# Performance work log

Measured on AMD Instinct MI355X. Metric: run time of the kernel, lower is better.

Reference implementation:

```python
import jax, jax.numpy as jnp
import numpy as np

RPE_LEN = 14  # rpe_length
HEADS = 10
HDIM = 64
EMBED = 640
DFF = 2560


def layer_norm(x, g, b, eps=1e-5):
    mu = jnp.mean(x, axis=-1, keepdims=True)
    var = jnp.var(x, axis=-1, keepdims=True)
    return (x - mu) * jax.lax.rsqrt(var + eps) * g + b


def rpe_embeddings(table_v, table_h, N):
    """RelativePosition2D.forward(N, N) -> [N, N, head_dim]."""
    L = N - 1
    s = int(L ** 0.5)  # 14 for N=197
    r = jnp.arange(L)
    dist_v = r[None, :] // s - r[:, None] // s
    dist_h = r[None, :] % s - r[:, None] % s
    idx_v = jnp.clip(dist_v, -RPE_LEN, RPE_LEN) + RPE_LEN + 1
    idx_h = jnp.clip(dist_h, -RPE_LEN, RPE_LEN) + RPE_LEN + 1
    # pad one row/col of zeros at the front (class token -> index 0)
    idx_v = jnp.pad(idx_v, ((1, 0), (1, 0)))
    idx_h = jnp.pad(idx_h, ((1, 0), (1, 0)))
    return table_v[idx_v] + table_h[idx_h]


def setup_inputs() -> dict:
    key = jax.random.key(0)
    ks = jax.random.split(key, 20)
    B, N, E, H, D, F = 64, 197, EMBED, HEADS, HDIM, DFF
    T = 2 * RPE_LEN + 2  # 30
    std = 0.02
    return {
        "x": jax.random.normal(ks[0], (B, N, E), jnp.float32),
        "ln1_g": jnp.ones((E,), jnp.float32),
        "ln1_b": jnp.zeros((E,), jnp.float32),
        "Wq": jax.random.normal(ks[1], (H * D, E), jnp.float32) * std,
        "Wk": jax.random.normal(ks[2], (H * D, E), jnp.float32) * std,
        "Wv": jax.random.normal(ks[3], (H * D, E), jnp.float32) * std,
        "Wp": jax.random.normal(ks[4], (E, H * D), jnp.float32) * std,
        "bp": jnp.zeros((E,), jnp.float32),
        "rpk_v": jax.random.normal(ks[5], (T, D), jnp.float32) * std,
        "rpk_h": jax.random.normal(ks[6], (T, D), jnp.float32) * std,
        "rpv_v": jax.random.normal(ks[7], (T, D), jnp.float32) * std,
        "rpv_h": jax.random.normal(ks[8], (T, D), jnp.float32) * std,
        "ln2_g": jnp.ones((E,), jnp.float32),
        "ln2_b": jnp.zeros((E,), jnp.float32),
        "W1": jax.random.normal(ks[9], (F, E), jnp.float32) * std,
        "b1": jnp.zeros((F,), jnp.float32),
        "W2": jax.random.normal(ks[10], (E, F), jnp.float32) * std,
        "b2": jnp.zeros((E,), jnp.float32),
    }


def reference(x, ln1_g, ln1_b, Wq, Wk, Wv, Wp, bp,
              rpk_v, rpk_h, rpv_v, rpv_h,
              ln2_g, ln2_b, W1, b1, W2, b2):
    B, N, E = x.shape
    H, D = HEADS, HDIM
    scale = D ** (-0.5)

    # --- attention block (pre-norm) ---
    residual = x
    h = layer_norm(x, ln1_g, ln1_b)
    q = (h @ Wq.T).reshape(B, N, H, D)
    k = (h @ Wk.T).reshape(B, N, H, D)
    v = (h @ Wv.T).reshape(B, N, H, D)

    attn = jnp.einsum('bnhd,bmhd->bhnm', q, k) * scale
    r_p_k = rpe_embeddings(rpk_v, rpk_h, N)          # [N, N, D]
    attn = attn + jnp.einsum('bnhd,nmd->bhnm', q, r_p_k) * scale
    attn = jax.nn.softmax(attn, axis=-1)

    o = jnp.einsum('bhnm,bmhd->bhnd', attn, v)
    r_p_v = rpe_embeddings(rpv_v, rpv_h, N)          # [N, N, D]
    o = o + jnp.einsum('bhnm,nmd->bhnd', attn, r_p_v)
    o = o.transpose(0, 2, 1, 3).reshape(B, N, H * D)
    x = residual + o @ Wp.T + bp

    # --- FFN block (pre-norm) ---
    residual = x
    h = layer_norm(x, ln2_g, ln2_b)
    h = jax.nn.gelu(h @ W1.T + b1, approximate=False)
    x = residual + h @ W2.T + b2
    return x
```

## Files before the change

kernel.cpp:

```cpp
#include <hip/hip_runtime.h>
#include <hip/hip_bf16.h>
#include <math.h>

#define NN   197
#define EE   640
#define HH   10
#define DD   64
#define FF   2560
#define MTOK (64 * 197)
#define RPE_T 30

typedef __hip_bfloat16 bf16;
typedef __attribute__((ext_vector_type(8))) __bf16 bf16x8;
typedef __attribute__((ext_vector_type(4))) float  floatx4;
typedef __attribute__((ext_vector_type(8))) unsigned short ushort8;

#define MFMA32(a, b, c) __builtin_amdgcn_mfma_f32_16x16x32_bf16(a, b, c, 0, 0, 0)

__device__ __forceinline__ float bfbits2f(unsigned short u) {
    union { unsigned int i; float f; } x; x.i = ((unsigned int)u) << 16; return x.f;
}
__device__ __forceinline__ unsigned short f2bf(float f) {
    bf16 t = __float2bfloat16(f);
    unsigned short u; __builtin_memcpy(&u, &t, 2); return u;
}
__device__ __forceinline__ void gld16(const bf16* g, bf16* l) {
    __builtin_amdgcn_global_load_lds(
        (const __attribute__((address_space(1))) unsigned int*)g,
        (__attribute__((address_space(3))) unsigned int*)l, 16, 0, 0);
}

__global__ void detect_kernel(const unsigned int* __restrict__ g, int* __restrict__ flag) {
    if (threadIdx.x == 0) flag[0] = (g[0] == 0x3F800000u) ? 1 : 0;
}

struct ConvDesc {
    const void* src[18];
    bf16*       dst[18];
    int         end8[18];
};

__global__ __launch_bounds__(256) void conv_fused(
    ConvDesc d, int total8, const int* __restrict__ flag)
{
    int c = blockIdx.x * 256 + threadIdx.x;
    if (c >= total8) return;
    int s = 0, start = 0;
#pragma unroll
    for (int i = 0; i < 17; ++i) {
        if (c >= d.end8[i]) { s = i + 1; start = d.end8[i]; }
    }
    int local = c - start;
    if (flag[0]) {
        const float* sp = (const float*)d.src[s] + (size_t)local * 8;
        bf16 t[8];
#pragma unroll
        for (int j = 0; j < 8; ++j) t[j] = __float2bfloat16(sp[j]);
        *(ushort8*)(d.dst[s] + (size_t)local * 8) = *(const ushort8*)t;
    } else {
        ((ushort8*)d.dst[s])[local] = ((const ushort8*)d.src[s])[local];
    }
}

__global__ __launch_bounds__(256) void rpetrans_kernel(
    const bf16* __restrict__ rvv, const bf16* __restrict__ rvh,
    unsigned short* __restrict__ rvvT, unsigned short* __restrict__ rvhT)
{
    int t = blockIdx.x * 256 + threadIdx.x;
    if (t < 64 * 32) {
        int d = t >> 5, tt = t & 31;
        rvvT[t] = (tt < RPE_T) ? ((const unsigned short*)rvv)[tt * 64 + d] : 0;
        rvhT[t] = (tt < RPE_T) ? ((const unsigned short*)rvh)[tt * 64 + d] : 0;
    }
}

__global__ __launch_bounds__(256) void vtrans_kernel(
    const bf16* __restrict__ qkv, unsigned short* __restrict__ VtG)
{
    int bh = blockIdx.x;
    int b = bh / HH, h = bh % HH;
    unsigned short* dst = VtG + (size_t)bh * (64 * 224);
    for (int t = threadIdx.x; t < 224 * 8; t += 256) {
        int m = t >> 3, d8 = (t & 7) << 3;
        ushort8 val = {0, 0, 0, 0, 0, 0, 0, 0};
        if (m < NN)
            val = *(const ushort8*)(qkv + ((size_t)b * NN + m) * 1920 + 1280 + h * 64 + d8);
#pragma unroll
        for (int j = 0; j < 8; ++j) dst[(d8 + j) * 224 + m] = val[j];
    }
}

__global__ __launch_bounds__(256) void ln_kernel(
    const void* __restrict__ xb, size_t xrow0, int xdyn,
    const int* __restrict__ flag,
    const bf16* __restrict__ g, const bf16* __restrict__ b,
    bf16* __restrict__ out, int nrows)
{
    int row  = blockIdx.x * 4 + (threadIdx.x >> 6);
    if (row >= nrows) return;
    int lane = threadIdx.x & 63;
    const int f32 = xdyn && flag[0];
    const size_t base = (xrow0 + row) * (size_t)EE;
    float vals[10];
    float s = 0.f, ss = 0.f;
#pragma unroll
    for (int j = 0; j < 10; ++j) {
        int e = j * 64 + lane;
        float f = f32 ? ((const float*)xb)[base + e]
                      : (float)((const bf16*)xb)[base + e];
        vals[j] = f; s += f; ss += f * f;
    }
#pragma unroll
    for (int off = 32; off; off >>= 1) {
        s  += __shfl_xor(s, off);
        ss += __shfl_xor(ss, off);
    }
    float mean = s * (1.f / EE);
    float var  = ss * (1.f / EE) - mean * mean;
    float rs   = rsqrtf(var + 1e-5f);
#pragma unroll
    for (int j = 0; j < 10; ++j) {
        int e = j * 64 + lane;
        float hv = (vals[j] - mean) * rs * (float)g[e] + (float)b[e];
        out[(size_t)row * EE + e] = __float2bfloat16(hv);
    }
}

__global__ __launch_bounds__(256) void gemm128(
    const bf16* __restrict__ A, const bf16* __restrict__ B,
    const bf16* __restrict__ bias,
    const void* __restrict__ residb, size_t resid_row0, int resid_dyn,
    void* __restrict__ outb, size_t out_row0, int out_dyn,
    const int* __restrict__ flag,
    int M, int N, int K, int gelu)
{
    __shared__ bf16 At[2][128 * 32];
    __shared__ bf16 Bt[2][128 * 32];

    const int tid  = threadIdx.x;
    const int wave = tid >> 6, lane = tid & 63;
    const int quad = lane >> 4, l16 = lane & 15;
    const int wy = wave >> 1, wx = wave & 1;
    const int n0 = blockIdx.x * 128;
    const int m0 = blockIdx.y * 128;

    const int drow   = wave * 16 + (lane >> 2);
    const int gchunk = ((lane & 3) ^ ((lane >> 3) & 3)) * 8;
    const int ar0 = min(m0 + drow, M - 1);
    const int ar1 = min(m0 + 64 + drow, M - 1);
    const bf16* Ag0 = A + (size_t)ar0 * K + gchunk;
    const bf16* Ag1 = A + (size_t)ar1 * K + gchunk;
    const bf16* Bg0 = B + (size_t)(n0 + drow) * K + gchunk;
    const bf16* Bg1 = B + (size_t)(n0 + 64 + drow) * K + gchunk;
    bf16* At00 = &At[0][wave * 512];
    bf16* At01 = &At[0][2048 + wave * 512];
    bf16* At10 = &At[1][wave * 512];
    bf16* At11 = &At[1][2048 + wave * 512];
    bf16* Bt00 = &Bt[0][wave * 512];
    bf16* Bt01 = &Bt[0][2048 + wave * 512];
    bf16* Bt10 = &Bt[1][wave * 512];
    bf16* Bt11 = &Bt[1][2048 + wave * 512];

    const int swz = (quad ^ ((l16 >> 1) & 3)) * 8;

    floatx4 acc[4][4] = {};

    for (int k0 = 0; k0 < K; k0 += 64) {
        __syncthreads();
        gld16(Ag0 + k0,      At00);
        gld16(Ag1 + k0,      At01);
        gld16(Ag0 + k0 + 32, At10);
        gld16(Ag1 + k0 + 32, At11);
        gld16(Bg0 + k0,      Bt00);
        gld16(Bg1 + k0,      Bt01);
        gld16(Bg0 + k0 + 32, Bt10);
        gld16(Bg1 + k0 + 32, Bt11);
        __syncthreads();

#pragma unroll
        for (int kk = 0; kk < 2; ++kk) {
            bf16x8 af[4], bfr[4];
#pragma unroll
            for (int s = 0; s < 4; ++s)
                af[s] = *(const bf16x8*)(&At[kk][(wy * 64 + s * 16 + l16) * 32 + swz]);
#pragma unroll
            for (int t = 0; t < 4; ++t)
                bfr[t] = *(const bf16x8*)(&Bt[kk][(wx * 64 + t * 16 + l16) * 32 + swz]);
#pragma unroll
            for (int s = 0; s < 4; ++s)
#pragma unroll
                for (int t = 0; t < 4; ++t)
                    acc[s][t] = MFMA32(af[s], bfr[t], acc[s][t]);
        }
    }

    const int fr = resid_dyn && flag[0];
    const int fo = out_dyn && flag[0];
    float bv[4];
#pragma unroll
    for (int t = 0; t < 4; ++t)
        bv[t] = bias ? (float)bias[n0 + wx * 64 + t * 16 + l16] : 0.f;

#pragma unroll
    for (int s = 0; s < 4; ++s) {
#pragma unroll
        for (int i = 0; i < 4; ++i) {
            int m = m0 + wy * 64 + s * 16 + quad * 4 + i;
            if (m < M) {
                size_t rowoff_o = (out_row0 + m) * (size_t)N;
                size_t rowoff_r = (resid_row0 + m) * (size_t)N;
#pragma unroll
                for (int t = 0; t < 4; ++t) {
                    int n = n0 + wx * 64 + t * 16 + l16;
                    float v = acc[s][t][i] + bv[t];
                    if (gelu) v = 0.5f * v * (1.f + erff(v * 0.70710678118f));
                    if (residb)
                        v += fr ? ((const float*)residb)[rowoff_r + n]
                                : (float)((const bf16*)residb)[rowoff_r + n];
                    if (fo) ((float*)outb)[rowoff_o + n] = v;
                    else    ((bf16*)outb)[rowoff_o + n]  = __float2bfloat16(v);
                }
            }
        }
    }
}

__global__ __launch_bounds__(256) void attn_kernel(
    const bf16* __restrict__ qkv,
    const bf16* __restrict__ tkv, const bf16* __restrict__ tkh,
    const unsigned short* __restrict__ rvvT,
    const unsigned short* __restrict__ rvhT,
    const unsigned short* __restrict__ VtG,
    bf16* __restrict__ o)
{
    __shared__ unsigned short Pm[64 * 232];
    __shared__ unsigned short PSv[64 * 40];
    __shared__ unsigned short PSh[64 * 40];
    __shared__ float QTv[64 * 32];
    __shared__ float QTh[64 * 32];

    const int tid  = threadIdx.x;
    const int wave = tid >> 6, lane = tid & 63;
    const int quad = lane >> 4, l16 = lane & 15;
    const int b  = blockIdx.x / HH, h = blockIdx.x % HH;
    const int qt = blockIdx.y;
    const size_t rowbase = (size_t)b * NN;

    for (int t = tid; t < 64 * 40; t += 256) { PSv[t] = 0; PSh[t] = 0; }
    for (int t = tid; t < 64 * 24; t += 256) Pm[(t / 24) * 232 + 208 + (t % 24)] = 0;
    __syncthreads();

    const int rA = qt * 64 + wave * 16 + l16;
    const bf16* qrow = qkv + (rowbase + min(rA, NN - 1)) * 1920 + h * 64;
    bf16x8 qa0 = *(const bf16x8*)(qrow + quad * 8);
    bf16x8 qa1 = *(const bf16x8*)(qrow + 32 + quad * 8);

    {
        floatx4 av[2] = {}, ah[2] = {};
#pragma unroll
        for (int ct = 0; ct < 2; ++ct) {
            int t = min(ct * 16 + l16, RPE_T - 1);
            av[ct] = MFMA32(qa0, *(const bf16x8*)(tkv + t * 64 + quad * 8), av[ct]);
            av[ct] = MFMA32(qa1, *(const bf16x8*)(tkv + t * 64 + 32 + quad * 8), av[ct]);
            ah[ct] = MFMA32(qa0, *(const bf16x8*)(tkh + t * 64 + quad * 8), ah[ct]);
            ah[ct] = MFMA32(qa1, *(const bf16x8*)(tkh + t * 64 + 32 + quad * 8), ah[ct]);
        }
#pragma unroll
        for (int ct = 0; ct < 2; ++ct)
#pragma unroll
            for (int i = 0; i < 4; ++i) {
                int row = wave * 16 + quad * 4 + i;
                QTv[row * 32 + ct * 16 + l16] = av[ct][i];
                QTh[row * 32 + ct * 16 + l16] = ah[ct][i];
            }
    }

    floatx4 sacc[13];
#pragma unroll
    for (int mt = 0; mt < 13; ++mt) {
        const bf16* krow = qkv + (rowbase + min(mt * 16 + l16, NN - 1)) * 1920
                           + 640 + h * 64;
        floatx4 a = {};
        a = MFMA32(qa0, *(const bf16x8*)(krow + quad * 8), a);
        a = MFMA32(qa1, *(const bf16x8*)(krow + 32 + quad * 8), a);
        sacc[mt] = a;
    }

    int nn4[4], jn4[4], in4[4];
#pragma unroll
    for (int i = 0; i < 4; ++i) {
        int n = qt * 64 + wave * 16 + quad * 4 + i;
        nn4[i] = n;
        jn4[i] = (n > 0) ? (n - 1) / 14 : 0;
        in4[i] = (n > 0) ? (n - 1) % 14 : 0;
    }
    float mx4[4] = {-3e38f, -3e38f, -3e38f, -3e38f};
#pragma unroll
    for (int mt = 0; mt < 13; ++mt) {
        int m = mt * 16 + l16;
        int jm = (m > 0) ? (m - 1) / 14 : 0;
        int im = (m > 0) ? (m - 1) % 14 : 0;
        bool mok = (m < NN);
#pragma unroll
        for (int i = 0; i < 4; ++i) {
            int row = wave * 16 + quad * 4 + i;
            int iv = (nn4[i] == 0 || m == 0) ? 0 : (jm - jn4[i] + 15);
            int ih = (nn4[i] == 0 || m == 0) ? 0 : (im - in4[i] + 15);
            float val = mok ? (sacc[mt][i] + QTv[row * 32 + iv] + QTh[row * 32 + ih]) * 0.125f
                            : -3e38f;
            sacc[mt][i] = val;
            mx4[i] = fmaxf(mx4[i], val);
        }
    }
#pragma unroll
    for (int i = 0; i < 4; ++i)
#pragma unroll
        for (int off = 1; off < 16; off <<= 1)
            mx4[i] = fmaxf(mx4[i], __shfl_xor(mx4[i], off));

    float sm4[4] = {0.f, 0.f, 0.f, 0.f};
#pragma unroll
    for (int mt = 0; mt < 13; ++mt) {
#pragma unroll
        for (int i = 0; i < 4; ++i) {
            float p = __expf(sacc[mt][i] - mx4[i]);
            sm4[i] += p;
            Pm[(wave * 16 + quad * 4 + i) * 232 + mt * 16 + l16] = f2bf(p);
        }
    }
#pragma unroll
    for (int i = 0; i < 4; ++i)
#pragma unroll
        for (int off = 1; off < 16; off <<= 1)
            sm4[i] += __shfl_xor(sm4[i], off);

    for (int t = lane; t < 224; t += 64) {
        int rl = t / 14, j = t % 14;
        int row = wave * 16 + rl;
        int n = qt * 64 + row;
        if (n >= 1 && n < NN) {
            float aR = 0.f, aC = 0.f;
#pragma unroll
            for (int u = 0; u < 14; ++u) {
                aR += bfbits2f(Pm[row * 232 + 1 + j * 14 + u]);
                aC += bfbits2f(Pm[row * 232 + 1 + u * 14 + j]);
            }
            int jn2 = (n - 1) / 14, in2 = (n - 1) % 14;
            PSv[row * 40 + (j - jn2 + 15)] = f2bf(aR);
            PSh[row * 40 + (j - in2 + 15)] = f2bf(aC);
        }
    }
    if (lane < 16) {
        int row = wave * 16 + lane;
        int n = qt * 64 + row;
        if (n < NN) {
            float p0 = (n == 0) ? sm4[0] : bfbits2f(Pm[row * 232]);
            PSv[row * 40] = f2bf(p0);
            PSh[row * 40] = f2bf(p0);
        }
    }

    floatx4 oacc[4] = {};
    {
        bf16x8 pav = *(const bf16x8*)(const void*)&PSv[(wave * 16 + l16) * 40 + quad * 8];
        bf16x8 pah = *(const bf16x8*)(const void*)&PSh[(wave * 16 + l16) * 40 + quad * 8];
#pragma unroll
        for (int ct = 0; ct < 4; ++ct) {
            bf16x8 bv  = *(const bf16x8*)(const void*)&rvvT[(ct * 16 + l16) * 32 + quad * 8];
            bf16x8 bh2 = *(const bf16x8*)(const void*)&rvhT[(ct * 16 + l16) * 32 + quad * 8];
            oacc[ct] = MFMA32(pav, bv,  oacc[ct]);
            oacc[ct] = MFMA32(pah, bh2, oacc[ct]);
        }
    }
    const unsigned short* vt = VtG + (size_t)blockIdx.x * (64 * 224);
    for (int k0 = 0; k0 < 224; k0 += 32) {
        bf16x8 pa = *(const bf16x8*)(const void*)&Pm[(wave * 16 + l16) * 232 + k0 + quad * 8];
#pragma unroll
        for (int ct = 0; ct < 4; ++ct) {
            bf16x8 vb = *(const bf16x8*)(const void*)&vt[(ct * 16 + l16) * 224 + k0 + quad * 8];
            oacc[ct] = MFMA32(pa, vb, oacc[ct]);
        }
    }
#pragma unroll
    for (int i = 0; i < 4; ++i) {
        float rinv = 1.f / sm4[i];
        int row = wave * 16 + quad * 4 + i;
        int n = qt * 64 + row;
        if (n < NN) {
#pragma unroll
            for (int ct = 0; ct < 4; ++ct)
                o[(rowbase + n) * 640 + h * 64 + ct * 16 + l16] =
                    __float2bfloat16(oacc[ct][i] * rinv);
        }
    }
}

extern "C" void kernel_launch(void* const* d_in, const int* in_sizes, int n_in,
                              void* d_out, int out_size, void* d_ws, size_t ws_size,
                              hipStream_t stream)
{
    char* ws = (char*)d_ws;
    size_t off = 0;
    auto alloc = [&](size_t bytes) -> void* {
        void* p = ws + off;
        off += (bytes + 255) & ~(size_t)255;
        return p;
    };

    int* flag = (int*)alloc(256);
    bf16* xc   = (bf16*)alloc((size_t)MTOK * EE * 2);
    bf16* Wqc  = (bf16*)alloc((size_t)EE * EE * 2);
    bf16* Wkc  = (bf16*)alloc((size_t)EE * EE * 2);
    bf16* Wvc  = (bf16*)alloc((size_t)EE * EE * 2);
    bf16* Wpc  = (bf16*)alloc((size_t)EE * EE * 2);
    bf16* W1c  = (bf16*)alloc((size_t)FF * EE * 2);
    bf16* W2c  = (bf16*)alloc((size_t)EE * FF * 2);
    bf16* l1g  = (bf16*)alloc(EE * 2);
    bf16* l1b  = (bf16*)alloc(EE * 2);
    bf16* l2g  = (bf16*)alloc(EE * 2);
    bf16* l2b  = (bf16*)alloc(EE * 2);
    bf16* bpc  = (bf16*)alloc(EE * 2);
    bf16* b1c  = (bf16*)alloc(FF * 2);
    bf16* b2c  = (bf16*)alloc(EE * 2);
    bf16* rkv  = (bf16*)alloc(RPE_T * DD * 2);
    bf16* rkh  = (bf16*)alloc(RPE_T * DD * 2);
    bf16* rvv  = (bf16*)alloc(RPE_T * DD * 2);
    bf16* rvh  = (bf16*)alloc(RPE_T * DD * 2);
    unsigned short* rvvT = (unsigned short*)alloc(64 * 32 * 2);
    unsigned short* rvhT = (unsigned short*)alloc(64 * 32 * 2);
    const size_t cvt_end = off;

    int Bc = 0;
    const int cands[6] = {64, 32, 16, 8, 4, 2};
    for (int i = 0; i < 6; ++i) {
        size_t rows = (size_t)NN * cands[i];
        size_t need = cvt_end + rows * 10240 + (size_t)cands[i] * HH * 64 * 224 * 2 + 8192;
        if (need <= ws_size) { Bc = cands[i]; break; }
    }
    if (Bc == 0) return;

    const int nchunks = 64 / Bc;
    const int rows    = NN * Bc;
    bf16* h1   = (bf16*)alloc((size_t)rows * EE * 2);
    bf16* qkvb = (bf16*)alloc((size_t)rows * 1920 * 2);
    bf16* h3   = (bf16*)alloc((size_t)rows * FF * 2);
    unsigned short* VtG = (unsigned short*)alloc((size_t)Bc * HH * 64 * 224 * 2);

    detect_kernel<<<1, 64, 0, stream>>>((const unsigned int*)d_in[1], flag);
    {
        ConvDesc cd;
        const void* srcs[18] = { d_in[0], d_in[3], d_in[4], d_in[5], d_in[6],
                                 d_in[14], d_in[16], d_in[1], d_in[2], d_in[12],
                                 d_in[13], d_in[7], d_in[15], d_in[17], d_in[8],
                                 d_in[9], d_in[10], d_in[11] };
        bf16* dsts[18] = { xc, Wqc, Wkc, Wvc, Wpc, W1c, W2c, l1g, l1b, l2g,
                           l2b, bpc, b1c, b2c, rkv, rkh, rvv, rvh };
        int ns[18] = { MTOK * EE, EE * EE, EE * EE, EE * EE, EE * EE, FF * EE,
                       EE * FF, EE, EE, EE, EE, EE, FF, EE,
                       RPE_T * DD, RPE_T * DD, RPE_T * DD, RPE_T * DD };
        int cum = 0;
        for (int i = 0; i < 18; ++i) {
            cd.src[i] = srcs[i]; cd.dst[i] = dsts[i];
            cum += ns[i] / 8; cd.end8[i] = cum;
        }
        conv_fused<<<(cum + 255) / 256, 256, 0, stream>>>(cd, cum, flag);
    }
    rpetrans_kernel<<<8, 256, 0, stream>>>(rvv, rvh, rvvT, rvhT);

    const int gM128 = (rows + 127) / 128;
    const int gLN   = (rows + 3) / 4;

    for (int c = 0; c < nchunks; ++c) {
        const size_t row0 = (size_t)c * rows;

        ln_kernel<<<gLN, 256, 0, stream>>>(xc, row0, 0, flag, l1g, l1b, h1, rows);

        gemm128<<<dim3(1920 / 128, gM128), 256, 0, stream>>>(
            h1, Wqc, nullptr, nullptr, 0, 0, qkvb, 0, 0, flag, rows, 1920, EE, 0);

        vtrans_kernel<<<Bc * HH, 256, 0, stream>>>(qkvb, VtG);

        attn_kernel<<<dim3(Bc * HH, 4), 256, 0, stream>>>(
            qkvb, rkv, rkh, rvvT, rvhT, VtG, h1);

        gemm128<<<dim3(EE / 128, gM128), 256, 0, stream>>>(
            h1, Wpc, bpc, xc, row0, 0, d_out, row0, 1, flag, rows, EE, EE, 0);
    }

    for (int c = 0; c < nchunks; ++c) {
        const size_t row0 = (size_t)c * rows;

        ln_kernel<<<gLN, 256, 0, stream>>>(d_out, row0, 1, flag, l2g, l2b, h1, rows);

        gemm128<<<dim3(FF / 128, gM128), 256, 0, stream>>>(
            h1, W1c, b1c, nullptr, 0, 0, h3, 0, 0, flag, rows, FF, EE, 1);

        gemm128<<<dim3(EE / 128, gM128), 256, 0, stream>>>(
            h3, W2c, b2c, d_out, row0, 1, d_out, row0, 1, flag, rows, EE, FF, 0);
    }
}
```

Baseline: 503.5 us.

## Compute RPE value sums via MFMA selection matrices, tanh GELU, swap GEMM grid order

Replaces the scalar row/column summation of attention probabilities (used for the relative-position value term) with MFMA products against precomputed 0/1 selection matrices, fused into the P·V loop. Stores the Q·RPE-key tables in bf16 instead of fp32 in shared memory. Swaps the exact erf GELU for a tanh approximation built on exp. Swaps the GEMM grid axes so M tiles vary fastest, changing L2 reuse of weight tiles. The tanh GELU and the bf16 tables add approximation error.

```diff
diff --git a/kernel.cpp b/kernel.cpp
--- a/kernel.cpp
+++ b/kernel.cpp
@@ -29,6 +29,14 @@
         (const __attribute__((address_space(1))) unsigned int*)g,
         (__attribute__((address_space(3))) unsigned int*)l, 16, 0, 0);
 }
+__device__ __forceinline__ float gelu_f(float v) {
+    float y = 0.7978845608f * (v + 0.044715f * v * v * v);
+    float a = fabsf(y);
+    float e = __expf(-2.f * a);
+    float t = (1.f - e) / (1.f + e);
+    t = (y < 0.f) ? -t : t;
+    return 0.5f * v * (1.f + t);
+}
 
 __global__ void detect_kernel(const unsigned int* __restrict__ g, int* __restrict__ flag) {
     if (threadIdx.x == 0) flag[0] = (g[0] == 0x3F800000u) ? 1 : 0;
@@ -71,6 +79,18 @@
         int d = t >> 5, tt = t & 31;
         rvvT[t] = (tt < RPE_T) ? ((const unsigned short*)rvv)[tt * 64 + d] : 0;
         rvhT[t] = (tt < RPE_T) ? ((const unsigned short*)rvh)[tt * 64 + d] : 0;
+    }
+}
+
+__global__ __launch_bounds__(256) void selbuild_kernel(
+    bf16* __restrict__ SelV, bf16* __restrict__ SelH)
+{
+    int t = blockIdx.x * 256 + threadIdx.x;
+    if (t < 16 * 224) {
+        int j = t / 224, m = t % 224;
+        bool valid = (j < 14) && (m >= 1) && (m < 197);
+        SelV[t] = __float2bfloat16((valid && (m - 1) / 14 == j) ? 1.f : 0.f);
+        SelH[t] = __float2bfloat16((valid && (m - 1) % 14 == j) ? 1.f : 0.f);
     }
 }
 
@@ -141,8 +161,8 @@
     const int wave = tid >> 6, lane = tid & 63;
     const int quad = lane >> 4, l16 = lane & 15;
     const int wy = wave >> 1, wx = wave & 1;
-    const int n0 = blockIdx.x * 128;
-    const int m0 = blockIdx.y * 128;
+    const int m0 = blockIdx.x * 128;
+    const int n0 = blockIdx.y * 128;
 
     const int drow   = wave * 16 + (lane >> 2);
     const int gchunk = ((lane & 3) ^ ((lane >> 3) & 3)) * 8;
@@ -213,7 +233,7 @@
                 for (int t = 0; t < 4; ++t) {
                     int n = n0 + wx * 64 + t * 16 + l16;
                     float v = acc[s][t][i] + bv[t];
-                    if (gelu) v = 0.5f * v * (1.f + erff(v * 0.70710678118f));
+                    if (gelu) v = gelu_f(v);
                     if (residb)
                         v += fr ? ((const float*)residb)[rowoff_r + n]
                                 : (float)((const bf16*)residb)[rowoff_r + n];
@@ -231,13 +251,14 @@
     const unsigned short* __restrict__ rvvT,
     const unsigned short* __restrict__ rvhT,
     const unsigned short* __restrict__ VtG,
+    const bf16* __restrict__ SelV, const bf16* __restrict__ SelH,
     bf16* __restrict__ o)
 {
     __shared__ unsigned short Pm[64 * 232];
     __shared__ unsigned short PSv[64 * 40];
     __shared__ unsigned short PSh[64 * 40];
-    __shared__ float QTv[64 * 32];
-    __shared__ float QTh[64 * 32];
+    __shared__ unsigned short QTv[64 * 32];
+    __shared__ unsigned short QTh[64 * 32];
 
     const int tid  = threadIdx.x;
     const int wave = tid >> 6, lane = tid & 63;
@@ -270,8 +291,8 @@
 #pragma unroll
             for (int i = 0; i < 4; ++i) {
                 int row = wave * 16 + quad * 4 + i;
-                QTv[row * 32 + ct * 16 + l16] = av[ct][i];
-                QTh[row * 32 + ct * 16 + l16] = ah[ct][i];
+                QTv[row * 32 + ct * 16 + l16] = f2bf(av[ct][i]);
+                QTh[row * 32 + ct * 16 + l16] = f2bf(ah[ct][i]);
             }
     }
 
@@ -306,7 +327,8 @@
             int row = wave * 16 + quad * 4 + i;
             int iv = (nn4[i] == 0 || m == 0) ? 0 : (jm - jn4[i] + 15);
             int ih = (nn4[i] == 0 || m == 0) ? 0 : (im - in4[i] + 15);
-            float val = mok ? (sacc[mt][i] + QTv[row * 32 + iv] + QTh[row * 32 + ih]) * 0.125f
+            float val = mok ? (sacc[mt][i] + bfbits2f(QTv[row * 32 + iv])
+                               + bfbits2f(QTh[row * 32 + ih])) * 0.125f
                             : -3e38f;
             sacc[mt][i] = val;
             mx4[i] = fmaxf(mx4[i], val);
@@ -334,20 +356,28 @@
         for (int off = 1; off < 16; off <<= 1)
             sm4[i] += __shfl_xor(sm4[i], off);
 
-    for (int t = lane; t < 224; t += 64) {
-        int rl = t / 14, j = t % 14;
-        int row = wave * 16 + rl;
+    floatx4 oacc[4] = {};
+    floatx4 psv = {}, psh = {};
+    const unsigned short* vt = VtG + (size_t)blockIdx.x * (64 * 224);
+    for (int k0 = 0; k0 < 224; k0 += 32) {
+        bf16x8 pa = *(const bf16x8*)(const void*)&Pm[(wave * 16 + l16) * 232 + k0 + quad * 8];
+#pragma unroll
+        for (int ct = 0; ct < 4; ++ct) {
+            bf16x8 vb = *(const bf16x8*)(const void*)&vt[(ct * 16 + l16) * 224 + k0 + quad * 8];
+            oacc[ct] = MFMA32(pa, vb, oacc[ct]);
+        }
+        psv = MFMA32(pa, *(const bf16x8*)(SelV + l16 * 224 + k0 + quad * 8), psv);
+        psh = MFMA32(pa, *(const bf16x8*)(SelH + l16 * 224 + k0 + quad * 8), psh);
+    }
+
+#pragma unroll
+    for (int i = 0; i < 4; ++i) {
+        int row = wave * 16 + quad * 4 + i;
         int n = qt * 64 + row;
-        if (n >= 1 && n < NN) {
-            float aR = 0.f, aC = 0.f;
-#pragma unroll
-            for (int u = 0; u < 14; ++u) {
-                aR += bfbits2f(Pm[row * 232 + 1 + j * 14 + u]);
-                aC += bfbits2f(Pm[row * 232 + 1 + u * 14 + j]);
-            }
+        if (n >= 1 && n < NN && l16 < 14) {
             int jn2 = (n - 1) / 14, in2 = (n - 1) % 14;
-            PSv[row * 40 + (j - jn2 + 15)] = f2bf(aR);
-            PSh[row * 40 + (j - in2 + 15)] = f2bf(aC);
+            PSv[row * 40 + (l16 - jn2 + 15)] = f2bf(psv[i]);
+            PSh[row * 40 + (l16 - in2 + 15)] = f2bf(psh[i]);
         }
     }
     if (lane < 16) {
@@ -360,7 +390,6 @@
         }
     }
 
-    floatx4 oacc[4] = {};
     {
         bf16x8 pav = *(const bf16x8*)(const void*)&PSv[(wave * 16 + l16) * 40 + quad * 8];
         bf16x8 pah = *(const bf16x8*)(const void*)&PSh[(wave * 16 + l16) * 40 + quad * 8];
@@ -370,15 +399,6 @@
             bf16x8 bh2 = *(const bf16x8*)(const void*)&rvhT[(ct * 16 + l16) * 32 + quad * 8];
             oacc[ct] = MFMA32(pav, bv,  oacc[ct]);
             oacc[ct] = MFMA32(pah, bh2, oacc[ct]);
-        }
-    }
-    const unsigned short* vt = VtG + (size_t)blockIdx.x * (64 * 224);
-    for (int k0 = 0; k0 < 224; k0 += 32) {
-        bf16x8 pa = *(const bf16x8*)(const void*)&Pm[(wave * 16 + l16) * 232 + k0 + quad * 8];
-#pragma unroll
-        for (int ct = 0; ct < 4; ++ct) {
-            bf16x8 vb = *(const bf16x8*)(const void*)&vt[(ct * 16 + l16) * 224 + k0 + quad * 8];
-            oacc[ct] = MFMA32(pa, vb, oacc[ct]);
         }
     }
 #pragma unroll
@@ -428,6 +448,8 @@
     bf16* rvh  = (bf16*)alloc(RPE_T * DD * 2);
     unsigned short* rvvT = (unsigned short*)alloc(64 * 32 * 2);
     unsigned short* rvhT = (unsigned short*)alloc(64 * 32 * 2);
+    bf16* SelV = (bf16*)alloc(16 * 224 * 2);
+    bf16* SelH = (bf16*)alloc(16 * 224 * 2);
     const size_t cvt_end = off;
 
     int Bc = 0;
@@ -466,6 +488,7 @@
         conv_fused<<<(cum + 255) / 256, 256, 0, stream>>>(cd, cum, flag);
     }
     rpetrans_kernel<<<8, 256, 0, stream>>>(rvv, rvh, rvvT, rvhT);
+    selbuild_kernel<<<14, 256, 0, stream>>>(SelV, SelH);
 
     const int gM128 = (rows + 127) / 128;
     const int gLN   = (rows + 3) / 4;
@@ -475,15 +498,15 @@
 
         ln_kernel<<<gLN, 256, 0, stream>>>(xc, row0, 0, flag, l1g, l1b, h1, rows);
 
-        gemm128<<<dim3(1920 / 128, gM128), 256, 0, stream>>>(
+        gemm128<<<dim3(gM128, 1920 / 128), 256, 0, stream>>>(
             h1, Wqc, nullptr, nullptr, 0, 0, qkvb, 0, 0, flag, rows, 1920, EE, 0);
 
         vtrans_kernel<<<Bc * HH, 256, 0, stream>>>(qkvb, VtG);
 
         attn_kernel<<<dim3(Bc * HH, 4), 256, 0, stream>>>(
-            qkvb, rkv, rkh, rvvT, rvhT, VtG, h1);
-
-        gemm128<<<dim3(EE / 128, gM128), 256, 0, stream>>>(
+            qkvb, rkv, rkh, rvvT, rvhT, VtG, SelV, SelH, h1);
+
+        gemm128<<<dim3(gM128, EE / 128), 256, 0, stream>>>(
             h1, Wpc, bpc, xc, row0, 0, d_out, row0, 1, flag, rows, EE, EE, 0);
     }
 
@@ -492,10 +515,10 @@
 
         ln_kernel<<<gLN, 256, 0, stream>>>(d_out, row0, 1, flag, l2g, l2b, h1, rows);
 
-        gemm128<<<dim3(FF / 128, gM128), 256, 0, stream>>>(
+        gemm128<<<dim3(gM128, FF / 128), 256, 0, stream>>>(
             h1, W1c, b1c, nullptr, 0, 0, h3, 0, 0, flag, rows, FF, EE, 1);
 
-        gemm128<<<dim3(EE / 128, gM128), 256, 0, stream>>>(
+        gemm128<<<dim3(gM128, EE / 128), 256, 0, stream>>>(
             h3, W2c, b2c, d_out, row0, 1, d_out, row0, 1, flag, rows, EE, FF, 0);
     }
 }
```

New measurement: 507.9 us. No clear change (+0.9%).
